# Performance work log

Measured on AMD Instinct MI355X. Metric: run time of the kernel, lower is better.

The kernel has to match this reference:

```python
import jax, jax.numpy as jnp
import numpy as np

EPS = 1.1920929e-07  # torch.finfo(float32).eps, used by nn.RMSNorm when eps=None
H = 16  # num_heads


def rmsnorm(x, w):
    return x * jax.lax.rsqrt(jnp.mean(x * x, axis=-1, keepdims=True) + EPS) * w


def attention(x, wq, wk, wv, wo, mask):
    # x: [b, s, d]; mask: [s, s] bool (True = attend)
    b, s, d = x.shape
    hd = d // H
    split = lambda t: t.reshape(b, s, H, hd).transpose(0, 2, 1, 3)  # b h s hd
    q, k, v = split(x @ wq), split(x @ wk), split(x @ wv)
    scale = 1.0 / float(np.sqrt(hd))
    scores = jnp.einsum('bhqd,bhkd->bhqk', q, k) * scale
    scores = jnp.where(mask, scores, jnp.asarray(-1e30, scores.dtype))
    p = jax.nn.softmax(scores, axis=-1)
    o = jnp.einsum('bhqk,bhkd->bhqd', p, v)
    return o.transpose(0, 2, 1, 3).reshape(b, s, d) @ wo


def setup_inputs() -> dict:
    key = jax.random.key(0)
    B, S, D, DFF = 2, 1024, 1024, 4096
    ks = jax.random.split(key, 32)
    w = lambda k, shape: jax.random.normal(k, shape, jnp.float32) * 0.02

    idx = jnp.arange(S)
    col_id = idx % 32            # COLUMN: interleaved column groups
    feat_id = idx // 128         # FEATURE: contiguous feature groups
    col_mask = col_id[:, None] == col_id[None, :]
    feat_mask = feat_id[:, None] == feat_id[None, :]
    nbr_mask = jnp.abs(idx[:, None] - idx[None, :]) <= 64  # NEIGHBOR: local band
    full_mask = jnp.ones((S, S), dtype=bool)

    return {
        'x': jax.random.normal(ks[0], (B, S, D), jnp.float32),
        'col_mask': col_mask, 'feat_mask': feat_mask,
        'nbr_mask': nbr_mask, 'full_mask': full_mask,
        'norm_c': jnp.ones((D,), jnp.float32), 'wq_c': w(ks[1], (D, D)), 'wk_c': w(ks[2], (D, D)), 'wv_c': w(ks[3], (D, D)), 'wo_c': w(ks[4], (D, D)),
        'norm_f': jnp.ones((D,), jnp.float32), 'wq_f': w(ks[5], (D, D)), 'wk_f': w(ks[6], (D, D)), 'wv_f': w(ks[7], (D, D)), 'wo_f': w(ks[8], (D, D)),
        'norm_n': jnp.ones((D,), jnp.float32), 'wq_n': w(ks[9], (D, D)), 'wk_n': w(ks[10], (D, D)), 'wv_n': w(ks[11], (D, D)), 'wo_n': w(ks[12], (D, D)),
        'norm_u': jnp.ones((D,), jnp.float32), 'wq_u': w(ks[13], (D, D)), 'wk_u': w(ks[14], (D, D)), 'wv_u': w(ks[15], (D, D)), 'wo_u': w(ks[16], (D, D)),
        'norm_ffn': jnp.ones((D,), jnp.float32), 'w_up': w(ks[17], (D, DFF)), 'w_gate': w(ks[18], (D, DFF)), 'w_down': w(ks[19], (DFF, D)),
    }


def reference(x, col_mask, feat_mask, nbr_mask, full_mask,
              norm_c, wq_c, wk_c, wv_c, wo_c,
              norm_f, wq_f, wk_f, wv_f, wo_f,
              norm_n, wq_n, wk_n, wv_n, wo_n,
              norm_u, wq_u, wk_u, wv_u, wo_u,
              norm_ffn, w_up, w_gate, w_down):
    x = x + attention(rmsnorm(x, norm_c), wq_c, wk_c, wv_c, wo_c, col_mask)
    x = x + attention(rmsnorm(x, norm_f), wq_f, wk_f, wv_f, wo_f, feat_mask)
    x = x + attention(rmsnorm(x, norm_n), wq_n, wk_n, wv_n, wo_n, nbr_mask)
    x = x + attention(rmsnorm(x, norm_u), wq_u, wk_u, wv_u, wo_u, full_mask)
    h = rmsnorm(x, norm_ffn)
    x = x + (jax.nn.silu(h @ w_gate) * (h @ w_up)) @ w_down  # SwiGLU FFN
    return x
```

## Files before the change

kernel.cpp:

```cpp
#include <hip/hip_runtime.h>
#include <math.h>
#include <stdint.h>


typedef __attribute__((ext_vector_type(8))) short bf16x8;
typedef __attribute__((ext_vector_type(4))) float f32x4;
typedef unsigned short ushort_t;
typedef unsigned int uint_t;

#define DEV static __device__ __forceinline__

DEV float bf2f(ushort_t u) { union { uint_t i; float f; } v; v.i = ((uint_t)u) << 16; return v.f; }
DEV ushort_t f2bf(float f) {
  union { float f; uint_t i; } v; v.f = f;
  uint_t r = v.i + 0x7fffu + ((v.i >> 16) & 1u);
  return (ushort_t)(r >> 16);
}
DEV uint_t pk2(ushort_t a, ushort_t b) { return (uint_t)a | ((uint_t)b << 16); }

DEV void gld16(const ushort_t* g, ushort_t* l) {
  __builtin_amdgcn_global_load_lds((const __attribute__((address_space(1))) void*)g,
                                   (__attribute__((address_space(3))) void*)l, 16, 0, 0);
}

struct Src16 { const float* p[16]; };

__global__ __launch_bounds__(256) void transpose16(Src16 s, ushort_t* __restrict__ qkvT,
                                                   ushort_t* __restrict__ woT) {
  __shared__ float tile[32][33];
  const int mz = blockIdx.z;
  const float* __restrict__ src = s.p[mz];
  const int l = mz >> 2, which = mz & 3;
  ushort_t* dst = (which < 3) ? (qkvT + (size_t)l*3072*1024 + (size_t)which*1024*1024)
                              : (woT  + (size_t)l*1024*1024);
  const int tx = threadIdx.x & 31, ty = threadIdx.x >> 5;
  const int r0 = blockIdx.y*32, c0 = blockIdx.x*32;
#pragma unroll
  for (int i = 0; i < 4; i++) tile[ty + 8*i][tx] = src[(size_t)(r0 + ty + 8*i)*1024 + c0 + tx];
  __syncthreads();
#pragma unroll
  for (int i = 0; i < 4; i++) dst[(size_t)(c0 + ty + 8*i)*1024 + r0 + tx] = f2bf(tile[tx][ty + 8*i]);
}

__global__ __launch_bounds__(256) void transpose_cvt(const float* __restrict__ src,
    ushort_t* __restrict__ dst, int R, int C, int row_off) {
  __shared__ float tile[32][33];
  const int tx = threadIdx.x & 31, ty = threadIdx.x >> 5;
  const int r0 = blockIdx.y*32, c0 = blockIdx.x*32;
#pragma unroll
  for (int i = 0; i < 4; i++) tile[ty + 8*i][tx] = src[(size_t)(r0 + ty + 8*i)*C + c0 + tx];
  __syncthreads();
#pragma unroll
  for (int i = 0; i < 4; i++)
    dst[(size_t)(row_off + c0 + ty + 8*i)*R + r0 + tx] = f2bf(tile[tx][ty + 8*i]);
}

__global__ __launch_bounds__(256) void copy_f32(const float* __restrict__ src,
                                                float* __restrict__ dst) {
  const size_t i = (size_t)blockIdx.x*256 + threadIdx.x;
  ((float4*)dst)[i] = ((const float4*)src)[i];
}

__global__ __launch_bounds__(256) void rmsnorm_k(const float* __restrict__ x,
    const float* __restrict__ w, ushort_t* __restrict__ out) {
  const int row = blockIdx.x, t = threadIdx.x;
  const float4 v = ((const float4*)(x + (size_t)row*1024))[t];
  float ss = v.x*v.x + v.y*v.y + v.z*v.z + v.w*v.w;
#pragma unroll
  for (int m = 32; m; m >>= 1) ss += __shfl_xor(ss, m);
  __shared__ float red[4];
  if ((t & 63) == 0) red[t >> 6] = ss;
  __syncthreads();
  const float tot = red[0] + red[1] + red[2] + red[3];
  const float rs = rsqrtf(tot * (1.0f/1024.0f) + 1.1920929e-07f);
  const float4 wv = ((const float4*)w)[t];
  uint2 o;
  o.x = pk2(f2bf(v.x*rs*wv.x), f2bf(v.y*rs*wv.y));
  o.y = pk2(f2bf(v.z*rs*wv.z), f2bf(v.w*rs*wv.w));
  *(uint2*)&out[(size_t)row*1024 + t*4] = o;
}

template<int BM, int BN, int EPI, int SPLITK>
__global__ __launch_bounds__(256, 2) void gemm_bt(
    const ushort_t* __restrict__ A, const ushort_t* __restrict__ BT,
    void* __restrict__ Cout, int M, int N, int K) {
  constexpr int BK = 64;
  __shared__ ushort_t Al[BM*BK];
  __shared__ ushort_t Bl[BN*BK];
  const int t = threadIdx.x, lane = t & 63;
  const int l15 = lane & 15, l4 = lane >> 4;
  int bid = blockIdx.y * gridDim.x + blockIdx.x;
  const int nwg = gridDim.x * gridDim.y;
  if ((nwg & 7) == 0) bid = (bid & 7) * (nwg >> 3) + (bid >> 3);
  const int n0 = (bid % gridDim.x) * BN;
  const int m0 = (bid / gridDim.x) * BM;
  constexpr int WM = BM/2, WN = BN/2, FM = WM/16, FN = WN/16;
  const int wm = ((t >> 6) >> 1) * WM;
  const int wn = ((t >> 6) & 1) * WN;
  const f32x4 zf = {0.f, 0.f, 0.f, 0.f};
  f32x4 acc[FM][FN];
#pragma unroll
  for (int m = 0; m < FM; m++)
#pragma unroll
    for (int n = 0; n < FN; n++) acc[m][n] = zf;
  constexpr int CA = (BM*BK)/(256*8), CB = (BN*BK)/(256*8);
  const int kz = blockIdx.z * (K / SPLITK);
  const int sw = l15 & 7;
  for (int k0 = kz; k0 < kz + K / SPLITK; k0 += BK) {
#pragma unroll
    for (int i = 0; i < CA; i++) {
      const int c = i*256 + t, row = c >> 3, ch = (c & 7) ^ (row & 7);
      gld16(&A[(size_t)(m0 + row)*K + k0 + ch*8], &Al[c*8]);
    }
#pragma unroll
    for (int i = 0; i < CB; i++) {
      const int c = i*256 + t, row = c >> 3, ch = (c & 7) ^ (row & 7);
      gld16(&BT[(size_t)(n0 + row)*K + k0 + ch*8], &Bl[c*8]);
    }
    __syncthreads();
#pragma unroll
    for (int kc = 0; kc < BK; kc += 32) {
      bf16x8 af[FM], bfr[FN];
#pragma unroll
      for (int m = 0; m < FM; m++)
        af[m] = *(const bf16x8*)&Al[(wm + m*16 + l15)*BK + (((kc >> 3) + l4) ^ sw)*8];
#pragma unroll
      for (int n = 0; n < FN; n++)
        bfr[n] = *(const bf16x8*)&Bl[(wn + n*16 + l15)*BK + (((kc >> 3) + l4) ^ sw)*8];
#pragma unroll
      for (int m = 0; m < FM; m++)
#pragma unroll
        for (int n = 0; n < FN; n++)
          acc[m][n] = __builtin_amdgcn_mfma_f32_16x16x32_bf16(af[m], bfr[n], acc[m][n], 0, 0, 0);
    }
    __syncthreads();
  }
#pragma unroll
  for (int m = 0; m < FM; m++)
#pragma unroll
    for (int n = 0; n < FN; n++)
#pragma unroll
      for (int r = 0; r < 4; r++) {
        const int row = m0 + wm + m*16 + l4*4 + r;
        const int col = n0 + wn + n*16 + l15;
        const size_t idx = (size_t)row*N + col;
        const float v = acc[m][n][r];
        if (EPI == 0) ((ushort_t*)Cout)[idx] = f2bf(v);
        else          atomicAdd(&((float*)Cout)[idx], v);
      }
}

__global__ __launch_bounds__(256) void attn_col_k(const ushort_t* __restrict__ qkv,
                                                  ushort_t* __restrict__ O) {
  __shared__ float Qs[32][65], Ks[32][65], Vs[32][65], P[32][33];
  const int c = blockIdx.x, h = blockIdx.y, b = blockIdx.z, t = threadIdx.x;
  const size_t base = (size_t)b*1024*3072 + h*64;
  for (int e = t; e < 2048; e += 256) {
    const int u = e >> 6, d = e & 63;
    const size_t rb = base + (size_t)(c + 32*u)*3072 + d;
    Qs[u][d] = bf2f(qkv[rb]);
    Ks[u][d] = bf2f(qkv[rb + 1024]);
    Vs[u][d] = bf2f(qkv[rb + 2048]);
  }
  __syncthreads();
  const int u = t >> 3, kq = (t & 7)*4;
  float sc[4] = {0.f, 0.f, 0.f, 0.f};
  for (int d = 0; d < 64; d++) {
    const float q = Qs[u][d];
#pragma unroll
    for (int j = 0; j < 4; j++) sc[j] += q * Ks[kq + j][d];
  }
#pragma unroll
  for (int j = 0; j < 4; j++) P[u][kq + j] = sc[j] * 0.125f;
  __syncthreads();
  if (t < 32) {
    float mx = P[t][0];
    for (int j = 1; j < 32; j++) mx = fmaxf(mx, P[t][j]);
    float sum = 0.f;
    for (int j = 0; j < 32; j++) { const float p = __expf(P[t][j] - mx); P[t][j] = p; sum += p; }
    const float inv = 1.0f / sum;
    for (int j = 0; j < 32; j++) P[t][j] *= inv;
  }
  __syncthreads();
  const int dg = (t & 7)*8;
  float o[8] = {0.f,0.f,0.f,0.f,0.f,0.f,0.f,0.f};
  for (int k = 0; k < 32; k++) {
    const float p = P[u][k];
#pragma unroll
    for (int j = 0; j < 8; j++) o[j] += p * Vs[k][dg + j];
  }
  uint4 w4;
  w4.x = pk2(f2bf(o[0]), f2bf(o[1])); w4.y = pk2(f2bf(o[2]), f2bf(o[3]));
  w4.z = pk2(f2bf(o[4]), f2bf(o[5])); w4.w = pk2(f2bf(o[6]), f2bf(o[7]));
  *(uint4*)&O[(size_t)(b*1024 + c + 32*u)*1024 + h*64 + dg] = w4;
}

template<int MASK, int NSPLIT>
__global__ __launch_bounds__(256) void attn_flash_k(const ushort_t* __restrict__ qkv,
    ushort_t* __restrict__ O, float* __restrict__ Opart, float* __restrict__ MLpart) {
  constexpr int LP = 66;
  __shared__ ushort_t Kl[64*LP];
  __shared__ ushort_t Vt[64*LP];
  __shared__ ushort_t Pl[4][16*LP];
  const int t = threadIdx.x, lane = t & 63, wave = t >> 6;
  const int l15 = lane & 15, l4 = lane >> 4;
  const int qt = blockIdx.x, h = blockIdx.y;
  const int b = blockIdx.z / NSPLIT, sp = blockIdx.z % NSPLIT;
  const int q0 = qt*64;
  const size_t base = (size_t)b*1024*3072 + h*64;
  const int qrow = q0 + wave*16 + l15;
  const bf16x8 qf0 = *(const bf16x8*)&qkv[base + (size_t)qrow*3072 + l4*8];
  const bf16x8 qf1 = *(const bf16x8*)&qkv[base + (size_t)qrow*3072 + 32 + l4*8];
  int klo, khi;
  if (MASK == 0)      { klo = q0 & ~127; khi = klo + 128; }
  else if (MASK == 1) { klo = (q0 >= 64) ? q0 - 64 : 0; khi = (q0 + 128 < 1024) ? q0 + 128 : 1024; }
  else                { klo = sp * (1024/NSPLIT); khi = klo + 1024/NSPLIT; }
  const int kr = t >> 2, kd = (t & 3)*16;
  const int vk = lane,  vd = wave*16;
  const ushort_t* kptr = qkv + base + 1024 + (size_t)kr*3072 + kd;
  const ushort_t* vptr = qkv + base + 2048 + (size_t)vk*3072 + vd;
  bf16x8 kg0 = *(const bf16x8*)&kptr[(size_t)klo*3072];
  bf16x8 kg1 = *(const bf16x8*)&kptr[(size_t)klo*3072 + 8];
  bf16x8 vg0 = *(const bf16x8*)&vptr[(size_t)klo*3072];
  bf16x8 vg1 = *(const bf16x8*)&vptr[(size_t)klo*3072 + 8];
  const f32x4 zf = {0.f, 0.f, 0.f, 0.f};
  f32x4 of[4];
#pragma unroll
  for (int n = 0; n < 4; n++) of[n] = zf;
  float mrow[4], lrow[4];
#pragma unroll
  for (int r = 0; r < 4; r++) { mrow[r] = -INFINITY; lrow[r] = 0.f; }

  for (int kb = klo; kb < khi; kb += 64) {
    *(bf16x8*)&Kl[kr*LP + kd] = kg0;
    *(bf16x8*)&Kl[kr*LP + kd + 8] = kg1;
#pragma unroll
    for (int j = 0; j < 8; j++) Vt[(vd + j)*LP + vk] = (ushort_t)vg0[j];
#pragma unroll
    for (int j = 0; j < 8; j++) Vt[(vd + 8 + j)*LP + vk] = (ushort_t)vg1[j];
    __syncthreads();
    if (kb + 64 < khi) {
      kg0 = *(const bf16x8*)&kptr[(size_t)(kb+64)*3072];
      kg1 = *(const bf16x8*)&kptr[(size_t)(kb+64)*3072 + 8];
      vg0 = *(const bf16x8*)&vptr[(size_t)(kb+64)*3072];
      vg1 = *(const bf16x8*)&vptr[(size_t)(kb+64)*3072 + 8];
    }
    f32x4 sf[4];
    __builtin_amdgcn_s_setprio(1);
#pragma unroll
    for (int s = 0; s < 4; s++) {
      const bf16x8 k0 = *(const bf16x8*)&Kl[(s*16 + l15)*LP + l4*8];
      const bf16x8 k1 = *(const bf16x8*)&Kl[(s*16 + l15)*LP + 32 + l4*8];
      sf[s] = __builtin_amdgcn_mfma_f32_16x16x32_bf16(qf0, k0, zf, 0, 0, 0);
      sf[s] = __builtin_amdgcn_mfma_f32_16x16x32_bf16(qf1, k1, sf[s], 0, 0, 0);
    }
    __builtin_amdgcn_s_setprio(0);
    float sv[4][4], tmax[4];
#pragma unroll
    for (int r = 0; r < 4; r++) tmax[r] = -INFINITY;
#pragma unroll
    for (int s = 0; s < 4; s++)
#pragma unroll
      for (int r = 0; r < 4; r++) {
        float a = sf[s][r]*0.125f;
        if (MASK == 1) {
          const int d = (q0 + wave*16 + l4*4 + r) - (kb + s*16 + l15);
          if (d > 64 || d < -64) a = -INFINITY;
        }
        sv[s][r] = a;
        tmax[r] = fmaxf(tmax[r], a);
      }
#pragma unroll
    for (int mk = 1; mk < 16; mk <<= 1)
#pragma unroll
      for (int r = 0; r < 4; r++) tmax[r] = fmaxf(tmax[r], __shfl_xor(tmax[r], mk));
    float fac[4], psum[4];
#pragma unroll
    for (int r = 0; r < 4; r++) {
      const float mn = fmaxf(mrow[r], tmax[r]);
      psum[r] = 0.f;
      if (mn == -INFINITY) {
        fac[r] = 1.0f;
#pragma unroll
        for (int s = 0; s < 4; s++) Pl[wave][(l4*4 + r)*LP + s*16 + l15] = 0;
      } else {
        fac[r] = __expf(mrow[r] - mn);
        mrow[r] = mn;
#pragma unroll
        for (int s = 0; s < 4; s++) {
          const float p = __expf(sv[s][r] - mn);
          psum[r] += p;
          Pl[wave][(l4*4 + r)*LP + s*16 + l15] = f2bf(p);
        }
      }
    }
#pragma unroll
    for (int mk = 1; mk < 16; mk <<= 1)
#pragma unroll
      for (int r = 0; r < 4; r++) psum[r] += __shfl_xor(psum[r], mk);
#pragma unroll
    for (int r = 0; r < 4; r++) lrow[r] = lrow[r]*fac[r] + psum[r];
#pragma unroll
    for (int n = 0; n < 4; n++)
#pragma unroll
      for (int r = 0; r < 4; r++) of[n][r] *= fac[r];
    const bf16x8 pa0 = *(const bf16x8*)&Pl[wave][l15*LP + l4*8];
    const bf16x8 pa1 = *(const bf16x8*)&Pl[wave][l15*LP + 32 + l4*8];
    __builtin_amdgcn_s_setprio(1);
#pragma unroll
    for (int n = 0; n < 4; n++) {
      const bf16x8 v0 = *(const bf16x8*)&Vt[(n*16 + l15)*LP + l4*8];
      const bf16x8 v1 = *(const bf16x8*)&Vt[(n*16 + l15)*LP + 32 + l4*8];
      of[n] = __builtin_amdgcn_mfma_f32_16x16x32_bf16(pa0, v0, of[n], 0, 0, 0);
      of[n] = __builtin_amdgcn_mfma_f32_16x16x32_bf16(pa1, v1, of[n], 0, 0, 0);
    }
    __builtin_amdgcn_s_setprio(0);
    __syncthreads();
  }
  if (NSPLIT == 1) {
#pragma unroll
    for (int n = 0; n < 4; n++)
#pragma unroll
      for (int r = 0; r < 4; r++) {
        const int qg = q0 + wave*16 + l4*4 + r;
        O[(size_t)(b*1024 + qg)*1024 + h*64 + n*16 + l15] = f2bf(of[n][r] / lrow[r]);
      }
  } else {
#pragma unroll
    for (int r = 0; r < 4; r++) {
      const int qg = q0 + wave*16 + l4*4 + r;
      const size_t row = ((size_t)(sp*2 + b)*1024 + qg)*16 + h;
#pragma unroll
      for (int n = 0; n < 4; n++) Opart[row*64 + n*16 + l15] = of[n][r];
      if (l15 == 0) *(float2*)&MLpart[row*2] = make_float2(mrow[r], lrow[r]);
    }
  }
}

__global__ __launch_bounds__(256) void attn_merge_k(const float* __restrict__ Opart,
    const float* __restrict__ ML, ushort_t* __restrict__ O) {
  const int idx = blockIdx.x*256 + threadIdx.x;
  const int d8 = (idx & 7)*8;
  const int h  = (idx >> 3) & 15;
  const int q  = (idx >> 7) & 1023;
  const int b  = idx >> 17;
  const size_t r0 = ((size_t)b*1024 + q)*16 + h;
  const size_t r1 = ((size_t)(2 + b)*1024 + q)*16 + h;
  const float2 ml0 = *(const float2*)&ML[r0*2];
  const float2 ml1 = *(const float2*)&ML[r1*2];
  const float m = fmaxf(ml0.x, ml1.x);
  const float w0 = __expf(ml0.x - m), w1 = __expf(ml1.x - m);
  const float inv = 1.0f / (ml0.y*w0 + ml1.y*w1);
  const float4* o0 = (const float4*)&Opart[r0*64 + d8];
  const float4* o1 = (const float4*)&Opart[r1*64 + d8];
  ushort_t ob[8];
#pragma unroll
  for (int i = 0; i < 2; i++) {
    const float4 a = o0[i], c = o1[i];
    ob[i*4+0] = f2bf((a.x*w0 + c.x*w1)*inv);
    ob[i*4+1] = f2bf((a.y*w0 + c.y*w1)*inv);
    ob[i*4+2] = f2bf((a.z*w0 + c.z*w1)*inv);
    ob[i*4+3] = f2bf((a.w*w0 + c.w*w1)*inv);
  }
  uint4 w4;
  w4.x = pk2(ob[0], ob[1]); w4.y = pk2(ob[2], ob[3]);
  w4.z = pk2(ob[4], ob[5]); w4.w = pk2(ob[6], ob[7]);
  *(uint4*)&O[((size_t)b*1024 + q)*1024 + h*64 + d8] = w4;
}

__global__ __launch_bounds__(256) void swiglu_k(const ushort_t* __restrict__ gu,
                                                ushort_t* __restrict__ out) {
  const size_t idx = (size_t)blockIdx.x*256 + threadIdx.x;
  const size_t m = idx >> 9, j8 = (idx & 511) << 3;
  const bf16x8 g8 = *(const bf16x8*)&gu[m*8192 + j8];
  const bf16x8 u8 = *(const bf16x8*)&gu[m*8192 + 4096 + j8];
  ushort_t o[8];
#pragma unroll
  for (int i = 0; i < 8; i++) {
    const float g = bf2f((ushort_t)g8[i]);
    const float u = bf2f((ushort_t)u8[i]);
    o[i] = f2bf(u * g / (1.0f + __expf(-g)));
  }
  uint4 w4;
  w4.x = pk2(o[0], o[1]); w4.y = pk2(o[2], o[3]); w4.z = pk2(o[4], o[5]); w4.w = pk2(o[6], o[7]);
  *(uint4*)&out[m*4096 + j8] = w4;
}

extern "C" void kernel_launch(void* const* d_in, const int* in_sizes, int n_in,
                              void* d_out, int out_size, void* d_ws, size_t ws_size,
                              hipStream_t stream) {
  (void)in_sizes; (void)n_in; (void)out_size; (void)ws_size;
  const float* x_in = (const float*)d_in[0];
  const float* norm[5] = { (const float*)d_in[5], (const float*)d_in[10], (const float*)d_in[15],
                           (const float*)d_in[20], (const float*)d_in[25] };
  char* w = (char*)d_ws;
  auto alloc = [&](size_t bytes) { char* p = w; w += (bytes + 255) & ~(size_t)255; return p; };
  ushort_t* qkvT = (ushort_t*)alloc(4ull*3072*1024*2);
  ushort_t* woT  = (ushort_t*)alloc(4ull*1024*1024*2);
  ushort_t* guT  = (ushort_t*)alloc(8192ull*1024*2);
  ushort_t* dnT  = (ushort_t*)alloc(4096ull*1024*2);
  float*    xbuf = (float*)  alloc(2048ull*1024*4);
  ushort_t* xn   = (ushort_t*)alloc(2048ull*1024*2);
  ushort_t* qkv  = (ushort_t*)alloc(2048ull*3072*2);
  ushort_t* attO = (ushort_t*)alloc(2048ull*1024*2);
  ushort_t* gu   = (ushort_t*)alloc(2048ull*8192*2);
  ushort_t* hmid = (ushort_t*)alloc(2048ull*4096*2);
  float* Opart  = (float*)gu;
  float* MLpart = (float*)hmid;

  Src16 s;
  for (int l = 0; l < 4; l++) {
    s.p[l*4 + 0] = (const float*)d_in[6 + l*5];
    s.p[l*4 + 1] = (const float*)d_in[7 + l*5];
    s.p[l*4 + 2] = (const float*)d_in[8 + l*5];
    s.p[l*4 + 3] = (const float*)d_in[9 + l*5];
  }
  transpose16<<<dim3(32, 32, 16), 256, 0, stream>>>(s, qkvT, woT);
  transpose_cvt<<<dim3(128, 32), 256, 0, stream>>>((const float*)d_in[27], guT, 1024, 4096, 0);
  transpose_cvt<<<dim3(128, 32), 256, 0, stream>>>((const float*)d_in[26], guT, 1024, 4096, 4096);
  transpose_cvt<<<dim3(32, 128), 256, 0, stream>>>((const float*)d_in[28], dnT, 4096, 1024, 0);

  copy_f32<<<2048, 256, 0, stream>>>(x_in, xbuf);

  for (int l = 0; l < 4; l++) {
    rmsnorm_k<<<2048, 256, 0, stream>>>(xbuf, norm[l], xn);
    gemm_bt<128,128,0,1><<<dim3(3072/128, 2048/128), 256, 0, stream>>>(
        xn, qkvT + (size_t)l*3072*1024, qkv, 2048, 3072, 1024);
    if (l == 0)      attn_col_k         <<<dim3(32, 16, 2), 256, 0, stream>>>(qkv, attO);
    else if (l == 1) attn_flash_k<0,1>  <<<dim3(16, 16, 2), 256, 0, stream>>>(qkv, attO, nullptr, nullptr);
    else if (l == 2) attn_flash_k<1,1>  <<<dim3(16, 16, 2), 256, 0, stream>>>(qkv, attO, nullptr, nullptr);
    else {
      attn_flash_k<2,2><<<dim3(16, 16, 4), 256, 0, stream>>>(qkv, nullptr, Opart, MLpart);
      attn_merge_k<<<1024, 256, 0, stream>>>(Opart, MLpart, attO);
    }
    gemm_bt<128,64,2,2><<<dim3(1024/64, 2048/128, 2), 256, 0, stream>>>(
        attO, woT + (size_t)l*1024*1024, xbuf, 2048, 1024, 1024);
  }
  rmsnorm_k<<<2048, 256, 0, stream>>>(xbuf, norm[4], xn);
  gemm_bt<128,128,0,1><<<dim3(8192/128, 2048/128), 256, 0, stream>>>(xn, guT, gu, 2048, 8192, 1024);
  swiglu_k<<<4096, 256, 0, stream>>>(gu, hmid);
  copy_f32<<<2048, 256, 0, stream>>>(xbuf, (float*)d_out);
  gemm_bt<128,128,2,4><<<dim3(1024/128, 2048/128, 4), 256, 0, stream>>>(
      hmid, dnT, d_out, 2048, 1024, 4096);
}
```

Measured before the change: 579.7 us.

## Pack V transpose stores, widen full-attention split to 4, retune GEMM tiles

The V tile is now loaded as two adjacent key rows per thread, so the transposed LDS writes become packed 32-bit stores instead of scattered 16-bit stores. The full-mask attention layer is split four ways along keys, and the merge kernel is generalized over the split count. The QKV GEMM uses 64-row tiles, the output projection uses a split-K of 4, and the down projection uses 64-wide N tiles. All of this is meant to raise occupancy and parallelism on the smaller launches, at the cost of more partial-sum traffic and more atomic or merge work.

```diff
diff --git a/kernel.cpp b/kernel.cpp
--- a/kernel.cpp
+++ b/kernel.cpp
@@ -216,13 +216,13 @@
   else if (MASK == 1) { klo = (q0 >= 64) ? q0 - 64 : 0; khi = (q0 + 128 < 1024) ? q0 + 128 : 1024; }
   else                { klo = sp * (1024/NSPLIT); khi = klo + 1024/NSPLIT; }
   const int kr = t >> 2, kd = (t & 3)*16;
-  const int vk = lane,  vd = wave*16;
+  const int vk2 = (t & 31)*2, vd = (t >> 5)*8;
   const ushort_t* kptr = qkv + base + 1024 + (size_t)kr*3072 + kd;
-  const ushort_t* vptr = qkv + base + 2048 + (size_t)vk*3072 + vd;
+  const ushort_t* vptr = qkv + base + 2048 + (size_t)vk2*3072 + vd;
   bf16x8 kg0 = *(const bf16x8*)&kptr[(size_t)klo*3072];
   bf16x8 kg1 = *(const bf16x8*)&kptr[(size_t)klo*3072 + 8];
   bf16x8 vg0 = *(const bf16x8*)&vptr[(size_t)klo*3072];
-  bf16x8 vg1 = *(const bf16x8*)&vptr[(size_t)klo*3072 + 8];
+  bf16x8 vg1 = *(const bf16x8*)&vptr[(size_t)klo*3072 + 3072];
   const f32x4 zf = {0.f, 0.f, 0.f, 0.f};
   f32x4 of[4];
 #pragma unroll
@@ -235,15 +235,14 @@
     *(bf16x8*)&Kl[kr*LP + kd] = kg0;
     *(bf16x8*)&Kl[kr*LP + kd + 8] = kg1;
 #pragma unroll
-    for (int j = 0; j < 8; j++) Vt[(vd + j)*LP + vk] = (ushort_t)vg0[j];
-#pragma unroll
-    for (int j = 0; j < 8; j++) Vt[(vd + 8 + j)*LP + vk] = (ushort_t)vg1[j];
+    for (int j = 0; j < 8; j++)
+      *(uint_t*)&Vt[(vd + j)*LP + vk2] = pk2((ushort_t)vg0[j], (ushort_t)vg1[j]);
     __syncthreads();
     if (kb + 64 < khi) {
       kg0 = *(const bf16x8*)&kptr[(size_t)(kb+64)*3072];
       kg1 = *(const bf16x8*)&kptr[(size_t)(kb+64)*3072 + 8];
       vg0 = *(const bf16x8*)&vptr[(size_t)(kb+64)*3072];
-      vg1 = *(const bf16x8*)&vptr[(size_t)(kb+64)*3072 + 8];
+      vg1 = *(const bf16x8*)&vptr[(size_t)(kb+64)*3072 + 3072];
     }
     f32x4 sf[4];
     __builtin_amdgcn_s_setprio(1);
@@ -337,6 +336,7 @@
   }
 }
 
+template<int NS>
 __global__ __launch_bounds__(256) void attn_merge_k(const float* __restrict__ Opart,
     const float* __restrict__ ML, ushort_t* __restrict__ O) {
   const int idx = blockIdx.x*256 + threadIdx.x;
@@ -344,27 +344,32 @@
   const int h  = (idx >> 3) & 15;
   const int q  = (idx >> 7) & 1023;
   const int b  = idx >> 17;
-  const size_t r0 = ((size_t)b*1024 + q)*16 + h;
-  const size_t r1 = ((size_t)(2 + b)*1024 + q)*16 + h;
-  const float2 ml0 = *(const float2*)&ML[r0*2];
-  const float2 ml1 = *(const float2*)&ML[r1*2];
-  const float m = fmaxf(ml0.x, ml1.x);
-  const float w0 = __expf(ml0.x - m), w1 = __expf(ml1.x - m);
-  const float inv = 1.0f / (ml0.y*w0 + ml1.y*w1);
-  const float4* o0 = (const float4*)&Opart[r0*64 + d8];
-  const float4* o1 = (const float4*)&Opart[r1*64 + d8];
-  ushort_t ob[8];
-#pragma unroll
-  for (int i = 0; i < 2; i++) {
-    const float4 a = o0[i], c = o1[i];
-    ob[i*4+0] = f2bf((a.x*w0 + c.x*w1)*inv);
-    ob[i*4+1] = f2bf((a.y*w0 + c.y*w1)*inv);
-    ob[i*4+2] = f2bf((a.z*w0 + c.z*w1)*inv);
-    ob[i*4+3] = f2bf((a.w*w0 + c.w*w1)*inv);
+  size_t rs[NS];
+  float2 ml[NS];
+  float m = -INFINITY;
+#pragma unroll
+  for (int s = 0; s < NS; s++) {
+    rs[s] = ((size_t)(s*2 + b)*1024 + q)*16 + h;
+    ml[s] = *(const float2*)&ML[rs[s]*2];
+    m = fmaxf(m, ml[s].x);
+  }
+  float den = 0.f, ws[NS];
+#pragma unroll
+  for (int s = 0; s < NS; s++) { ws[s] = __expf(ml[s].x - m); den += ml[s].y * ws[s]; }
+  const float inv = 1.0f / den;
+  float acc[8] = {0,0,0,0,0,0,0,0};
+#pragma unroll
+  for (int s = 0; s < NS; s++) {
+    const float4* op = (const float4*)&Opart[rs[s]*64 + d8];
+    const float4 a = op[0], c = op[1];
+    acc[0] += a.x*ws[s]; acc[1] += a.y*ws[s]; acc[2] += a.z*ws[s]; acc[3] += a.w*ws[s];
+    acc[4] += c.x*ws[s]; acc[5] += c.y*ws[s]; acc[6] += c.z*ws[s]; acc[7] += c.w*ws[s];
   }
   uint4 w4;
-  w4.x = pk2(ob[0], ob[1]); w4.y = pk2(ob[2], ob[3]);
-  w4.z = pk2(ob[4], ob[5]); w4.w = pk2(ob[6], ob[7]);
+  w4.x = pk2(f2bf(acc[0]*inv), f2bf(acc[1]*inv));
+  w4.y = pk2(f2bf(acc[2]*inv), f2bf(acc[3]*inv));
+  w4.z = pk2(f2bf(acc[4]*inv), f2bf(acc[5]*inv));
+  w4.w = pk2(f2bf(acc[6]*inv), f2bf(acc[7]*inv));
   *(uint4*)&O[((size_t)b*1024 + q)*1024 + h*64 + d8] = w4;
 }
 
@@ -424,22 +429,22 @@
 
   for (int l = 0; l < 4; l++) {
     rmsnorm_k<<<2048, 256, 0, stream>>>(xbuf, norm[l], xn);
-    gemm_bt<128,128,0,1><<<dim3(3072/128, 2048/128), 256, 0, stream>>>(
+    gemm_bt<64,128,0,1><<<dim3(3072/128, 2048/64), 256, 0, stream>>>(
         xn, qkvT + (size_t)l*3072*1024, qkv, 2048, 3072, 1024);
     if (l == 0)      attn_col_k         <<<dim3(32, 16, 2), 256, 0, stream>>>(qkv, attO);
     else if (l == 1) attn_flash_k<0,1>  <<<dim3(16, 16, 2), 256, 0, stream>>>(qkv, attO, nullptr, nullptr);
     else if (l == 2) attn_flash_k<1,1>  <<<dim3(16, 16, 2), 256, 0, stream>>>(qkv, attO, nullptr, nullptr);
     else {
-      attn_flash_k<2,2><<<dim3(16, 16, 4), 256, 0, stream>>>(qkv, nullptr, Opart, MLpart);
-      attn_merge_k<<<1024, 256, 0, stream>>>(Opart, MLpart, attO);
-    }
-    gemm_bt<128,64,2,2><<<dim3(1024/64, 2048/128, 2), 256, 0, stream>>>(
+      attn_flash_k<2,4><<<dim3(16, 16, 8), 256, 0, stream>>>(qkv, nullptr, Opart, MLpart);
+      attn_merge_k<4><<<1024, 256, 0, stream>>>(Opart, MLpart, attO);
+    }
+    gemm_bt<128,64,2,4><<<dim3(1024/64, 2048/128, 4), 256, 0, stream>>>(
         attO, woT + (size_t)l*1024*1024, xbuf, 2048, 1024, 1024);
   }
   rmsnorm_k<<<2048, 256, 0, stream>>>(xbuf, norm[4], xn);
   gemm_bt<128,128,0,1><<<dim3(8192/128, 2048/128), 256, 0, stream>>>(xn, guT, gu, 2048, 8192, 1024);
   swiglu_k<<<4096, 256, 0, stream>>>(gu, hmid);
   copy_f32<<<2048, 256, 0, stream>>>(xbuf, (float*)d_out);
-  gemm_bt<128,128,2,4><<<dim3(1024/128, 2048/128, 4), 256, 0, stream>>>(
+  gemm_bt<128,64,2,4><<<dim3(1024/64, 2048/128, 4), 256, 0, stream>>>(
       hmid, dnT, d_out, 2048, 1024, 4096);
 }
```

Measured after the change: 610.5 us. 1.05x slower.
